# Kernel optimization log

Measured on AMD Instinct MI355X. Metric: run time of the kernel, lower is better.

The kernel has to match this reference:

```python
import jax, jax.numpy as jnp
import numpy as np

B, T, D = 1, 2048, 1024
HQ, HKV, HD = 16, 4, 64
G = HQ // HKV
E, TOPK, F = 8, 2, 2752
LB = 0.01
SCALE = HD ** -0.5


def setup_inputs() -> dict:
    key = jax.random.key(0)
    ks = jax.random.split(key, 12)
    s = 0.02
    return {
        "x": jax.random.normal(ks[0], (B, T, D), jnp.float32),
        "g1": jnp.ones((D,), jnp.float32),
        "g2": jnp.ones((D,), jnp.float32),
        "wq": jax.random.normal(ks[1], (D, HQ * HD), jnp.float32) * s,
        "wk": jax.random.normal(ks[2], (D, HKV * HD), jnp.float32) * s,
        "wv": jax.random.normal(ks[3], (D, HKV * HD), jnp.float32) * s,
        "wo": jax.random.normal(ks[4], (D, D), jnp.float32) * s,
        "gate_w": jax.random.normal(ks[5], (D, E), jnp.float32) * s,
        "we_gate": jax.random.normal(ks[6], (E, D, F), jnp.float32) * s,
        "we_up": jax.random.normal(ks[7], (E, D, F), jnp.float32) * s,
        "we_down": jax.random.normal(ks[8], (E, F, D), jnp.float32) * s,
    }


def _rmsnorm(x, g, eps=1e-6):
    return x * g * jax.lax.rsqrt(jnp.mean(x * x, axis=-1, keepdims=True) + eps)


def _rope(q, k):
    # q: [B,HQ,T,HD], k: [B,HKV,T,HD]; standard rotate-half RoPE
    pos = jnp.arange(T, dtype=jnp.float32)
    inv_freq = 1.0 / (10000.0 ** (jnp.arange(0, HD, 2, dtype=jnp.float32) / HD))
    ang = pos[:, None] * inv_freq[None, :]                  # [T, HD/2]
    cos = jnp.concatenate([jnp.cos(ang), jnp.cos(ang)], -1)  # [T, HD]
    sin = jnp.concatenate([jnp.sin(ang), jnp.sin(ang)], -1)

    def rot_half(x):
        x1, x2 = jnp.split(x, 2, axis=-1)
        return jnp.concatenate([-x2, x1], axis=-1)

    def apply(x):
        return x * cos + rot_half(x) * sin
    return apply(q), apply(k)


def _attention(x, g1, wq, wk, wv, wo):
    h = _rmsnorm(x, g1)
    q = (h @ wq).reshape(B, T, HQ, HD).transpose(0, 2, 1, 3)   # [B,HQ,T,HD]
    k = (h @ wk).reshape(B, T, HKV, HD).transpose(0, 2, 1, 3)  # [B,HKV,T,HD]
    v = (h @ wv).reshape(B, T, HKV, HD).transpose(0, 2, 1, 3)
    q, k = _rope(q, k)
    qg = q.reshape(B, HKV, G, T, HD)
    # grouped scores without materializing repeated K/V
    scores = jnp.einsum('bkgtd,bksd->bkgts', qg, k) * SCALE     # [B,HKV,G,T,T]
    causal = jnp.tril(jnp.ones((T, T), bool))
    scores = jnp.where(causal, scores, jnp.float32(-jnp.inf))
    w = jax.nn.softmax(scores, axis=-1)
    o = jnp.einsum('bkgts,bksd->bkgtd', w, v)                  # [B,HKV,G,T,HD]
    o = o.reshape(B, HQ, T, HD).transpose(0, 2, 1, 3).reshape(B, T, D)
    return o @ wo


def _moe(x, g2, gate_w, we_gate, we_up, we_down):
    h = _rmsnorm(x, g2).reshape(B * T, D)                      # [N,D]
    N = B * T
    logits = h @ gate_w                                        # [N,E]
    probs = jax.nn.softmax(logits, axis=-1)
    topv, topi = jax.lax.top_k(probs, TOPK)                    # [N,TOPK]
    topv = topv / (topv.sum(-1, keepdims=True) + 1e-8)
    # dense combine weights [N,E]: same math as masked per-expert dispatch
    combine = jnp.zeros((N, E), h.dtype).at[jnp.arange(N)[:, None], topi].add(topv)
    gh = jnp.einsum('nd,edf->enf', h, we_gate)
    up = jnp.einsum('nd,edf->enf', h, we_up)
    y = jnp.einsum('enf,efd->end', jax.nn.silu(gh) * up, we_down)
    out = jnp.einsum('end,ne->nd', y, combine).reshape(B, T, D)
    # load-balancing aux loss
    frac = jnp.zeros((E,), probs.dtype).at[topi.reshape(-1)].add(1.0) / (N * TOPK)
    load = probs.mean(axis=0)
    aux = LB * E * jnp.sum(frac * load)
    return out, aux


def reference(x, g1, g2, wq, wk, wv, wo, gate_w, we_gate, we_up, we_down):
    x = x + _attention(x, g1, wq, wk, wv, wo)
    moe_out, aux = _moe(x, g2, gate_w, we_gate, we_up, we_down)
    x = x + moe_out
    return x, aux
```

## Files before the change

kernel.cpp:

```cpp
#include <hip/hip_runtime.h>
#include <cstdint>

typedef __attribute__((ext_vector_type(8))) short short8;
typedef __attribute__((ext_vector_type(4))) float floatx4;
typedef __attribute__((ext_vector_type(4))) unsigned short ushort4v;
typedef unsigned short ushort;

#define T_LEN 2048
#define D_DIM 1024
#define HQn 16
#define HKVn 4
#define NE 8
#define FF 2752
#define NTOK 2048
#define NSLOT 4096
#define ATT_SCALE 0.125f
#define GATE_TPB 16

__device__ inline ushort f2bf(float f) {
  union { float f; unsigned int i; } v; v.f = f;
  unsigned int r = v.i + 0x7fffu + ((v.i >> 16) & 1u);
  return (ushort)(r >> 16);
}
__device__ inline float bf2f(ushort h) {
  union { unsigned int i; float f; } v; v.i = ((unsigned int)h) << 16;
  return v.f;
}
__device__ inline void split8(const float* v, short8& hi, short8& lo) {
#pragma unroll
  for (int i = 0; i < 8; i++) {
    ushort h = f2bf(v[i]);
    hi[i] = (short)h;
    lo[i] = (short)f2bf(v[i] - bf2f(h));
  }
}
__device__ inline floatx4 mfma16(short8 a, short8 b, floatx4 c) {
  return __builtin_amdgcn_mfma_f32_16x16x32_bf16(a, b, c, 0, 0, 0);
}
#define DMA16(g, l)                                                              \
  __builtin_amdgcn_global_load_lds((const __attribute__((address_space(1))) void*)(g), \
                                   (__attribute__((address_space(3))) void*)(l), 16, 0, 0)

__global__ __launch_bounds__(256) void k_cvtT(const float* __restrict__ src,
                                              ushort* __restrict__ dst, int R, int C) {
  __shared__ float tile[32][33];
  size_t sb = (size_t)blockIdx.z * R * C;
  const float* s = src + sb;
  ushort* d = dst + sb;
  int r0 = blockIdx.y * 32, c0 = blockIdx.x * 32;
  int tc = threadIdx.x & 31, tr = threadIdx.x >> 5;
#pragma unroll
  for (int i = 0; i < 4; i++)
    tile[tr + i * 8][tc] = s[(size_t)(r0 + tr + i * 8) * C + c0 + tc];
  __syncthreads();
#pragma unroll
  for (int i = 0; i < 4; i++) {
    int cc = tr + i * 8;
    d[(size_t)(c0 + cc) * R + r0 + tc] = f2bf(tile[tc][cc]);
  }
}

__global__ __launch_bounds__(256) void k_cvtT2(const float* __restrict__ src,
                                               ushort* __restrict__ dh,
                                               ushort* __restrict__ dl, int R, int C) {
  __shared__ float tile[32][33];
  int r0 = blockIdx.y * 32, c0 = blockIdx.x * 32;
  int tc = threadIdx.x & 31, tr = threadIdx.x >> 5;
#pragma unroll
  for (int i = 0; i < 4; i++)
    tile[tr + i * 8][tc] = src[(size_t)(r0 + tr + i * 8) * C + c0 + tc];
  __syncthreads();
#pragma unroll
  for (int i = 0; i < 4; i++) {
    int cc = tr + i * 8;
    float v = tile[tc][cc];
    ushort h = f2bf(v);
    dh[(size_t)(c0 + cc) * R + r0 + tc] = h;
    dl[(size_t)(c0 + cc) * R + r0 + tc] = f2bf(v - bf2f(h));
  }
}

__global__ __launch_bounds__(256) void k_rmsnorm2(const float* __restrict__ x,
                                                  const float* __restrict__ g,
                                                  ushort* __restrict__ oh,
                                                  ushort* __restrict__ ol) {
  int row = blockIdx.x;
  int t = threadIdx.x;
  const float4* x4 = (const float4*)(x + (size_t)row * D_DIM);
  float4 v = x4[t];
  float ss = v.x * v.x + v.y * v.y + v.z * v.z + v.w * v.w;
#pragma unroll
  for (int off = 32; off; off >>= 1) ss += __shfl_xor(ss, off, 64);
  __shared__ float red[4];
  if ((t & 63) == 0) red[t >> 6] = ss;
  __syncthreads();
  float tot = red[0] + red[1] + red[2] + red[3];
  float sc = rsqrtf(tot * (1.0f / D_DIM) + 1e-6f);
  const float4* g4 = (const float4*)g;
  float4 gv = g4[t];
  float vals[4] = {v.x * gv.x * sc, v.y * gv.y * sc, v.z * gv.z * sc, v.w * gv.w * sc};
  ushort4v h4, l4;
#pragma unroll
  for (int i = 0; i < 4; i++) {
    ushort h = f2bf(vals[i]);
    h4[i] = h;
    l4[i] = f2bf(vals[i] - bf2f(h));
  }
  *(ushort4v*)(oh + (size_t)row * D_DIM + t * 4) = h4;
  *(ushort4v*)(ol + (size_t)row * D_DIM + t * 4) = l4;
}

__global__ __launch_bounds__(256) void k_sgemm(const ushort* __restrict__ Ahg,
                                               const ushort* __restrict__ Alg,
                                               const ushort* __restrict__ Bhg,
                                               const ushort* __restrict__ Blg,
                                               float* __restrict__ C,
                                               const float* __restrict__ res,
                                               int N, int K) {
  __shared__ __align__(16) ushort Ah[2048], Al[2048], Bh[4096], Bl[4096];
  int tid = threadIdx.x;
  int m0 = blockIdx.y * 64, n0 = blockIdx.x * 128;
  int wave = tid >> 6, lane = tid & 63, quad = lane >> 4, l15 = lane & 15;
  int wm = (wave >> 1) * 32, wn = (wave & 1) * 64;
  floatx4 acc[2][4];
#pragma unroll
  for (int i = 0; i < 2; i++)
#pragma unroll
    for (int j = 0; j < 4; j++) acc[i][j] = (floatx4){0.f, 0.f, 0.f, 0.f};
  const ushort* src[6];
  ushort* dst[6];
  int srow = lane >> 2;
  int kc = ((lane & 3) ^ ((lane >> 3) & 3)) * 8;
#pragma unroll
  for (int j = 0; j < 6; j++) {
    int c = wave * 6 + j;
    if (c < 4) {
      src[j] = Ahg + (size_t)(m0 + c * 16 + srow) * K + kc;
      dst[j] = Ah + c * 512;
    } else if (c < 8) {
      src[j] = Alg + (size_t)(m0 + (c - 4) * 16 + srow) * K + kc;
      dst[j] = Al + (c - 4) * 512;
    } else if (c < 16) {
      src[j] = Bhg + (size_t)(n0 + (c - 8) * 16 + srow) * K + kc;
      dst[j] = Bh + (c - 8) * 512;
    } else {
      src[j] = Blg + (size_t)(n0 + (c - 16) * 16 + srow) * K + kc;
      dst[j] = Bl + (c - 16) * 512;
    }
  }
  for (int k0 = 0; k0 < K; k0 += 32) {
#pragma unroll
    for (int j = 0; j < 6; j++) DMA16(src[j] + k0, dst[j]);
    __syncthreads();
    short8 ah[2], al[2], bh[4], bl[4];
#pragma unroll
    for (int mt = 0; mt < 2; mt++) {
      int ar = wm + mt * 16 + l15;
      int sw = (quad ^ ((ar >> 1) & 3)) * 8;
      ah[mt] = *(short8*)&Ah[ar * 32 + sw];
      al[mt] = *(short8*)&Al[ar * 32 + sw];
    }
#pragma unroll
    for (int nt = 0; nt < 4; nt++) {
      int br = wn + nt * 16 + l15;
      int sw = (quad ^ ((br >> 1) & 3)) * 8;
      bh[nt] = *(short8*)&Bh[br * 32 + sw];
      bl[nt] = *(short8*)&Bl[br * 32 + sw];
    }
#pragma unroll
    for (int mt = 0; mt < 2; mt++)
#pragma unroll
      for (int nt = 0; nt < 4; nt++) {
        acc[mt][nt] = mfma16(ah[mt], bh[nt], acc[mt][nt]);
        acc[mt][nt] = mfma16(ah[mt], bl[nt], acc[mt][nt]);
        acc[mt][nt] = mfma16(al[mt], bh[nt], acc[mt][nt]);
      }
    __syncthreads();
  }
#pragma unroll
  for (int mt = 0; mt < 2; mt++) {
    int row = m0 + wm + mt * 16 + quad * 4;
#pragma unroll
    for (int nt = 0; nt < 4; nt++) {
      int col = n0 + wn + nt * 16 + l15;
#pragma unroll
      for (int r = 0; r < 4; r++) {
        float v = acc[mt][nt][r];
        if (res) v += res[(size_t)(row + r) * N + col];
        C[(size_t)(row + r) * N + col] = v;
      }
    }
  }
}

__global__ __launch_bounds__(256) void k_rope_cvt(const float* __restrict__ qkvf,
                                                  ushort* __restrict__ qhi,
                                                  ushort* __restrict__ qlo,
                                                  ushort* __restrict__ khi,
                                                  ushort* __restrict__ klo) {
  int t = blockIdx.x;
  const float* row = qkvf + (size_t)t * 1536;
  for (int it = threadIdx.x; it < (HQn + HKVn) * 32; it += 256) {
    int hh = it >> 5, i = it & 31;
    float inv = powf(10000.0f, -(float)i / 32.0f);
    float ang = (float)t * inv;
    float c = cosf(ang), s = sinf(ang);
    const float* p;
    ushort *dh, *dl;
    size_t base;
    if (hh < HQn) {
      p = row + hh * 64;
      base = ((size_t)hh * T_LEN + t) * 64;
      dh = qhi; dl = qlo;
    } else {
      int h2 = hh - HQn;
      p = row + 1024 + h2 * 64;
      base = ((size_t)h2 * T_LEN + t) * 64;
      dh = khi; dl = klo;
    }
    float a = p[i], b = p[i + 32];
    float v0 = a * c - b * s;
    float v1 = b * c + a * s;
    ushort h0 = f2bf(v0);
    dh[base + i] = h0;
    dl[base + i] = f2bf(v0 - bf2f(h0));
    ushort h1 = f2bf(v1);
    dh[base + i + 32] = h1;
    dl[base + i + 32] = f2bf(v1 - bf2f(h1));
  }
}

__global__ __launch_bounds__(256) void k_vT(const float* __restrict__ qkvf,
                                            ushort* __restrict__ vbth,
                                            ushort* __restrict__ vbtl) {
  __shared__ float tile[32][33];
  int t0 = blockIdx.x * 32;
  int dh = blockIdx.y;
  int col0 = 1280 + dh * 32;
  int tc = threadIdx.x & 31, tr = threadIdx.x >> 5;
#pragma unroll
  for (int i = 0; i < 4; i++)
    tile[tr + i * 8][tc] = qkvf[(size_t)(t0 + tr + i * 8) * 1536 + col0 + tc];
  __syncthreads();
#pragma unroll
  for (int i = 0; i < 4; i++) {
    int dd = tr + i * 8;
    float v = tile[tc][dd];
    ushort h = f2bf(v);
    size_t idx = (size_t)(dh * 32 + dd) * T_LEN + t0 + tc;
    vbth[idx] = h;
    vbtl[idx] = f2bf(v - bf2f(h));
  }
}

__global__ __launch_bounds__(256) void k_attn(const ushort* __restrict__ qhi,
                                              const ushort* __restrict__ qlo,
                                              const ushort* __restrict__ khi,
                                              const ushort* __restrict__ klo,
                                              const ushort* __restrict__ vbth,
                                              const ushort* __restrict__ vbtl,
                                              ushort* __restrict__ obh,
                                              ushort* __restrict__ obl) {
  __shared__ __align__(16) ushort Kh[4096], Kl[4096], Vh[4096], Vl[4096];
  __shared__ ushort Psh[4 * 16 * 72], Psl[4 * 16 * 72];
  int qh = blockIdx.y, kvh = qh >> 2;
  int tid = threadIdx.x, wave = tid >> 6, lane = tid & 63;
  int quad = lane >> 4, l15 = lane & 15;
  int sx = l15 >> 1;
  int rlb = lane >> 3;
  int csb = (lane & 7) ^ (lane >> 4);
#pragma unroll 1
  for (int hf = 0; hf < 2; hf++) {
    int xt = hf ? (31 - (int)blockIdx.x) : (int)blockIdx.x;
    int r0 = xt * 64;
    const ushort* qbh_ = qhi + ((size_t)qh * T_LEN + r0 + wave * 16 + l15) * 64;
    const ushort* qbl_ = qlo + ((size_t)qh * T_LEN + r0 + wave * 16 + l15) * 64;
    short8 aqh0 = *(const short8*)&qbh_[quad * 8];
    short8 aqh1 = *(const short8*)&qbh_[32 + quad * 8];
    short8 aql0 = *(const short8*)&qbl_[quad * 8];
    short8 aql1 = *(const short8*)&qbl_[32 + quad * 8];
    floatx4 oacc[4];
#pragma unroll
    for (int nt = 0; nt < 4; nt++) oacc[nt] = (floatx4){0.f, 0.f, 0.f, 0.f};
    float mrun[4], lrun[4];
#pragma unroll
    for (int r = 0; r < 4; r++) { mrun[r] = -INFINITY; lrun[r] = 0.f; }
    for (int cc = 0; cc <= xt; cc++) {
      __syncthreads();
      if (wave < 2) {
        const ushort* G = (wave == 0) ? khi : klo;
        ushort* L = (wave == 0) ? Kh : Kl;
        size_t rbase = (size_t)kvh * T_LEN + cc * 64;
#pragma unroll
        for (int i = 0; i < 8; i++) {
          int ch = csb ^ ((i & 1) * 4);
          DMA16(G + (rbase + i * 8 + rlb) * 64 + ch * 8, L + i * 512);
        }
      } else {
        const ushort* G = (wave == 2) ? vbth : vbtl;
        ushort* L = (wave == 2) ? Vh : Vl;
#pragma unroll
        for (int i = 0; i < 8; i++) {
          int ch = csb ^ ((i & 1) * 4);
          DMA16(G + ((size_t)(kvh * 64 + i * 8 + rlb)) * T_LEN + cc * 64 + ch * 8,
                L + i * 512);
        }
      }
      __syncthreads();
      floatx4 s[4];
#pragma unroll
      for (int nt = 0; nt < 4; nt++) {
        int row = nt * 16 + l15;
        short8 bh0 = *(short8*)&Kh[row * 64 + (quad ^ sx) * 8];
        short8 bh1 = *(short8*)&Kh[row * 64 + ((4 + quad) ^ sx) * 8];
        short8 bl0 = *(short8*)&Kl[row * 64 + (quad ^ sx) * 8];
        short8 bl1 = *(short8*)&Kl[row * 64 + ((4 + quad) ^ sx) * 8];
        floatx4 z = (floatx4){0.f, 0.f, 0.f, 0.f};
        z = mfma16(aqh0, bh0, z);
        z = mfma16(aqh1, bh1, z);
        z = mfma16(aqh0, bl0, z);
        z = mfma16(aqh1, bl1, z);
        z = mfma16(aql0, bh0, z);
        z = mfma16(aql1, bh1, z);
        s[nt] = z;
      }
      int rowg0 = r0 + wave * 16 + quad * 4;
#pragma unroll
      for (int nt = 0; nt < 4; nt++) {
        int colg = cc * 64 + nt * 16 + l15;
#pragma unroll
        for (int r = 0; r < 4; r++) {
          float v = s[nt][r] * ATT_SCALE;
          s[nt][r] = (colg > rowg0 + r) ? -INFINITY : v;
        }
      }
      float mnew[4], alpha[4], psum[4];
#pragma unroll
      for (int r = 0; r < 4; r++) {
        float mx = fmaxf(fmaxf(s[0][r], s[1][r]), fmaxf(s[2][r], s[3][r]));
#pragma unroll
        for (int off = 1; off < 16; off <<= 1) mx = fmaxf(mx, __shfl_xor(mx, off, 64));
        mnew[r] = fmaxf(mrun[r], mx);
        psum[r] = 0.f;
      }
#pragma unroll
      for (int nt = 0; nt < 4; nt++)
#pragma unroll
        for (int r = 0; r < 4; r++) {
          float p = __expf(s[nt][r] - mnew[r]);
          s[nt][r] = p;
          psum[r] += p;
        }
#pragma unroll
      for (int r = 0; r < 4; r++) {
        float ps = psum[r];
#pragma unroll
        for (int off = 1; off < 16; off <<= 1) ps += __shfl_xor(ps, off, 64);
        alpha[r] = __expf(mrun[r] - mnew[r]);
        lrun[r] = lrun[r] * alpha[r] + ps;
        mrun[r] = mnew[r];
      }
#pragma unroll
      for (int nt = 0; nt < 4; nt++)
#pragma unroll
        for (int r = 0; r < 4; r++) oacc[nt][r] *= alpha[r];
#pragma unroll
      for (int nt = 0; nt < 4; nt++)
#pragma unroll
        for (int r = 0; r < 4; r++) {
          float p = s[nt][r];
          ushort ph = f2bf(p);
          Psh[wave * 1152 + (quad * 4 + r) * 72 + nt * 16 + l15] = ph;
          Psl[wave * 1152 + (quad * 4 + r) * 72 + nt * 16 + l15] = f2bf(p - bf2f(ph));
        }
      short8 aph0 = *(short8*)&Psh[wave * 1152 + l15 * 72 + quad * 8];
      short8 aph1 = *(short8*)&Psh[wave * 1152 + l15 * 72 + 32 + quad * 8];
      short8 apl0 = *(short8*)&Psl[wave * 1152 + l15 * 72 + quad * 8];
      short8 apl1 = *(short8*)&Psl[wave * 1152 + l15 * 72 + 32 + quad * 8];
#pragma unroll
      for (int nt = 0; nt < 4; nt++) {
        int row = nt * 16 + l15;
        short8 bvh0 = *(short8*)&Vh[row * 64 + (quad ^ sx) * 8];
        short8 bvh1 = *(short8*)&Vh[row * 64 + ((4 + quad) ^ sx) * 8];
        short8 bvl0 = *(short8*)&Vl[row * 64 + (quad ^ sx) * 8];
        short8 bvl1 = *(short8*)&Vl[row * 64 + ((4 + quad) ^ sx) * 8];
        oacc[nt] = mfma16(aph0, bvh0, oacc[nt]);
        oacc[nt] = mfma16(aph1, bvh1, oacc[nt]);
        oacc[nt] = mfma16(aph0, bvl0, oacc[nt]);
        oacc[nt] = mfma16(aph1, bvl1, oacc[nt]);
        oacc[nt] = mfma16(apl0, bvh0, oacc[nt]);
        oacc[nt] = mfma16(apl1, bvh1, oacc[nt]);
      }
    }
#pragma unroll
    for (int nt = 0; nt < 4; nt++)
#pragma unroll
      for (int r = 0; r < 4; r++) {
        int rowg = r0 + wave * 16 + quad * 4 + r;
        float v = oacc[nt][r] / lrun[r];
        ushort h = f2bf(v);
        size_t idx = (size_t)rowg * D_DIM + qh * 64 + nt * 16 + l15;
        obh[idx] = h;
        obl[idx] = f2bf(v - bf2f(h));
      }
  }
}

__global__ __launch_bounds__(256) void k_gate(const float* __restrict__ x1,
                                              const float* __restrict__ g2,
                                              const float* __restrict__ gw,
                                              int* __restrict__ counts,
                                              int* __restrict__ ids,
                                              float* __restrict__ wts,
                                              float* __restrict__ load_sum) {
  __shared__ float lsum[NE];
  __shared__ int lcount[NE];
  __shared__ int lbase[NE];
  __shared__ int ltok[GATE_TPB * 2];
  __shared__ int lexp[GATE_TPB * 2];
  __shared__ float lwt[GATE_TPB * 2];
  int tid = threadIdx.x, wave = tid >> 6, lane = tid & 63;
  if (tid < NE) { lsum[tid] = 0.f; lcount[tid] = 0; }
  __syncthreads();
  int t0 = blockIdx.x * GATE_TPB;
#pragma unroll
  for (int tt = 0; tt < GATE_TPB / 4; tt++) {
    int tloc = tt * 4 + wave;
    int token = t0 + tloc;
    const float* xp = x1 + (size_t)token * D_DIM;
    float acc[NE] = {};
    float ss = 0.f;
    for (int d = lane; d < D_DIM; d += 64) {
      float xv = xp[d];
      ss += xv * xv;
      float hv = xv * g2[d];
#pragma unroll
      for (int e = 0; e < NE; e++) acc[e] += hv * gw[d * NE + e];
    }
#pragma unroll
    for (int off = 32; off; off >>= 1) ss += __shfl_xor(ss, off, 64);
#pragma unroll
    for (int e = 0; e < NE; e++)
#pragma unroll
      for (int off = 32; off; off >>= 1) acc[e] += __shfl_xor(acc[e], off, 64);
    if (lane == 0) {
      float sc = rsqrtf(ss * (1.0f / D_DIM) + 1e-6f);
      float mx = -1e30f;
#pragma unroll
      for (int e = 0; e < NE; e++) { acc[e] *= sc; mx = fmaxf(mx, acc[e]); }
      float p[NE], sum = 0.f;
#pragma unroll
      for (int e = 0; e < NE; e++) { p[e] = expf(acc[e] - mx); sum += p[e]; }
#pragma unroll
      for (int e = 0; e < NE; e++) p[e] /= sum;
      int i1 = 0;
#pragma unroll
      for (int e = 1; e < NE; e++) if (acc[e] > acc[i1]) i1 = e;
      int i2 = (i1 == 0) ? 1 : 0;
#pragma unroll
      for (int e = 0; e < NE; e++) if (e != i1 && acc[e] > acc[i2]) i2 = e;
      float denom = p[i1] + p[i2] + 1e-8f;
      int slot = tloc * 2;
      lexp[slot] = i1; ltok[slot] = token; lwt[slot] = p[i1] / denom;
      lexp[slot + 1] = i2; ltok[slot + 1] = token; lwt[slot + 1] = p[i2] / denom;
      atomicAdd(&lcount[i1], 1);
      atomicAdd(&lcount[i2], 1);
#pragma unroll
      for (int e = 0; e < NE; e++) atomicAdd(&lsum[e], p[e]);
    }
  }
  __syncthreads();
  if (tid < NE) {
    lbase[tid] = atomicAdd(&counts[tid], lcount[tid]);
    atomicAdd(&load_sum[tid], lsum[tid]);
    lcount[tid] = 0;
  }
  __syncthreads();
  if (tid < GATE_TPB * 2) {
    int e = lexp[tid];
    int off = atomicAdd(&lcount[e], 1);
    int pos = lbase[e] + off;
    ids[e * NTOK + pos] = ltok[tid];
    wts[e * NTOK + pos] = lwt[tid];
  }
}

__global__ void k_offsets(const int* __restrict__ counts, int* __restrict__ offsets) {
  if (threadIdx.x == 0 && blockIdx.x == 0) {
    int s = 0;
    for (int e = 0; e < NE; e++) { offsets[e] = s; s += counts[e]; }
  }
}

__global__ __launch_bounds__(256) void k_moe_gateup(const ushort* __restrict__ h,
                                                    const ushort* __restrict__ wgT,
                                                    const ushort* __restrict__ wuT,
                                                    const int* __restrict__ ids,
                                                    const float* __restrict__ wts,
                                                    const int* __restrict__ counts,
                                                    const int* __restrict__ offsets,
                                                    ushort* __restrict__ act) {
  int e = blockIdx.z;
  int cnt = counts[e];
  int m0 = blockIdx.y * 128;
  if (m0 >= cnt) return;
  int n0 = blockIdx.x * 64;
  __shared__ __align__(16) ushort As[4096], Bg[2048], Bu[2048];
  __shared__ int toks[128];
  __shared__ float wrow[128];
  int tid = threadIdx.x;
  if (tid < 128) {
    int mm = m0 + tid;
    toks[tid] = (mm < cnt) ? ids[e * NTOK + mm] : 0;
    wrow[tid] = (mm < cnt) ? wts[e * NTOK + mm] : 0.f;
  }
  __syncthreads();
  int wave = tid >> 6, lane = tid & 63, quad = lane >> 4, l15 = lane & 15;
  int wm = (wave >> 1) * 64, wn = (wave & 1) * 32;
  const ushort* Wg = wgT + (size_t)e * FF * D_DIM;
  const ushort* Wu = wuT + (size_t)e * FF * D_DIM;
  const ushort* src[4];
  ushort* dst[4];
  int srow = lane >> 2;
  int kc = ((lane & 3) ^ ((lane >> 3) & 3)) * 8;
#pragma unroll
  for (int j = 0; j < 4; j++) {
    int c = wave * 4 + j;
    if (c < 8) {
      src[j] = h + (size_t)toks[c * 16 + srow] * D_DIM + kc;
      dst[j] = As + c * 512;
    } else if (c < 12) {
      src[j] = Wg + (size_t)(n0 + (c - 8) * 16 + srow) * D_DIM + kc;
      dst[j] = Bg + (c - 8) * 512;
    } else {
      src[j] = Wu + (size_t)(n0 + (c - 12) * 16 + srow) * D_DIM + kc;
      dst[j] = Bu + (c - 12) * 512;
    }
  }
  floatx4 accg[4][2], accu[4][2];
#pragma unroll
  for (int i = 0; i < 4; i++)
#pragma unroll
    for (int j = 0; j < 2; j++) {
      accg[i][j] = (floatx4){0.f, 0.f, 0.f, 0.f};
      accu[i][j] = (floatx4){0.f, 0.f, 0.f, 0.f};
    }
  for (int k0 = 0; k0 < D_DIM; k0 += 32) {
#pragma unroll
    for (int j = 0; j < 4; j++) DMA16(src[j] + k0, dst[j]);
    __syncthreads();
    short8 aF[4], bgF[2], buF[2];
#pragma unroll
    for (int mt = 0; mt < 4; mt++) {
      int ar = wm + mt * 16 + l15;
      int sw = (quad ^ ((ar >> 1) & 3)) * 8;
      aF[mt] = *(short8*)&As[ar * 32 + sw];
    }
#pragma unroll
    for (int nt = 0; nt < 2; nt++) {
      int br = wn + nt * 16 + l15;
      int sw = (quad ^ ((br >> 1) & 3)) * 8;
      bgF[nt] = *(short8*)&Bg[br * 32 + sw];
      buF[nt] = *(short8*)&Bu[br * 32 + sw];
    }
#pragma unroll
    for (int mt = 0; mt < 4; mt++)
#pragma unroll
      for (int nt = 0; nt < 2; nt++) {
        accg[mt][nt] = mfma16(aF[mt], bgF[nt], accg[mt][nt]);
        accu[mt][nt] = mfma16(aF[mt], buF[nt], accu[mt][nt]);
      }
    __syncthreads();
  }
  int aoff = offsets[e];
#pragma unroll
  for (int mt = 0; mt < 4; mt++) {
    int mrow = wm + mt * 16 + quad * 4;
#pragma unroll
    for (int nt = 0; nt < 2; nt++) {
      int col = n0 + wn + nt * 16 + l15;
#pragma unroll
      for (int r = 0; r < 4; r++) {
        int ml = mrow + r;
        if (m0 + ml < cnt) {
          float g = accg[mt][nt][r];
          float u = accu[mt][nt][r];
          float sil = g / (1.f + __expf(-g));
          act[(size_t)(aoff + m0 + ml) * FF + col] = f2bf(sil * u * wrow[ml]);
        }
      }
    }
  }
}

__global__ __launch_bounds__(256) void k_moe_down(const ushort* __restrict__ act,
                                                  const ushort* __restrict__ wdT,
                                                  const int* __restrict__ ids,
                                                  const int* __restrict__ counts,
                                                  const int* __restrict__ offsets,
                                                  float* __restrict__ moe_acc) {
  int e = blockIdx.z & 7;
  int kh = blockIdx.z >> 3;
  int cnt = counts[e];
  int m0 = blockIdx.y * 128;
  if (m0 >= cnt) return;
  int n0 = blockIdx.x * 128;
  __shared__ __align__(16) ushort As[4096], Bs[4096];
  __shared__ int toks[128];
  int tid = threadIdx.x;
  if (tid < 128) {
    int mm = m0 + tid;
    toks[tid] = (mm < cnt) ? ids[e * NTOK + mm] : 0;
  }
  __syncthreads();
  int wave = tid >> 6, lane = tid & 63, quad = lane >> 4, l15 = lane & 15;
  int wm = (wave >> 1) * 64, wn = (wave & 1) * 64;
  int aoff = offsets[e];
  const ushort* Wd = wdT + (size_t)e * D_DIM * FF;
  const ushort* src[4];
  ushort* dst[4];
  int srow = lane >> 2;
  int kc = ((lane & 3) ^ ((lane >> 3) & 3)) * 8;
#pragma unroll
  for (int j = 0; j < 4; j++) {
    int c = wave * 4 + j;
    if (c < 8) {
      src[j] = act + (size_t)(aoff + m0 + c * 16 + srow) * FF + kc;
      dst[j] = As + c * 512;
    } else {
      src[j] = Wd + (size_t)(n0 + (c - 8) * 16 + srow) * FF + kc;
      dst[j] = Bs + (c - 8) * 512;
    }
  }
  floatx4 acc[4][4];
#pragma unroll
  for (int i = 0; i < 4; i++)
#pragma unroll
    for (int j = 0; j < 4; j++) acc[i][j] = (floatx4){0.f, 0.f, 0.f, 0.f};
  int kbeg = kh * 1376;
  for (int k0 = kbeg; k0 < kbeg + 1376; k0 += 32) {
#pragma unroll
    for (int j = 0; j < 4; j++) DMA16(src[j] + k0, dst[j]);
    __syncthreads();
    short8 aF[4], bF[4];
#pragma unroll
    for (int mt = 0; mt < 4; mt++) {
      int ar = wm + mt * 16 + l15;
      int sw = (quad ^ ((ar >> 1) & 3)) * 8;
      aF[mt] = *(short8*)&As[ar * 32 + sw];
    }
#pragma unroll
    for (int nt = 0; nt < 4; nt++) {
      int br = wn + nt * 16 + l15;
      int sw = (quad ^ ((br >> 1) & 3)) * 8;
      bF[nt] = *(short8*)&Bs[br * 32 + sw];
    }
#pragma unroll
    for (int mt = 0; mt < 4; mt++)
#pragma unroll
      for (int nt = 0; nt < 4; nt++) acc[mt][nt] = mfma16(aF[mt], bF[nt], acc[mt][nt]);
    __syncthreads();
  }
#pragma unroll
  for (int mt = 0; mt < 4; mt++) {
    int mrow = wm + mt * 16 + quad * 4;
#pragma unroll
    for (int nt = 0; nt < 4; nt++) {
      int col = n0 + wn + nt * 16 + l15;
#pragma unroll
      for (int r = 0; r < 4; r++) {
        int ml = mrow + r;
        if (m0 + ml < cnt)
          atomicAdd(&moe_acc[(size_t)toks[ml] * D_DIM + col], acc[mt][nt][r]);
      }
    }
  }
}

__global__ __launch_bounds__(256) void k_add(const float* __restrict__ a,
                                             const float* __restrict__ b,
                                             float* __restrict__ o) {
  int i = blockIdx.x * 256 + threadIdx.x;
  float4 va = ((const float4*)a)[i];
  float4 vb = ((const float4*)b)[i];
  float4 vo;
  vo.x = va.x + vb.x; vo.y = va.y + vb.y; vo.z = va.z + vb.z; vo.w = va.w + vb.w;
  ((float4*)o)[i] = vo;
}

__global__ void k_aux(const int* __restrict__ counts, const float* __restrict__ load_sum,
                      float* __restrict__ out_aux) {
  if (threadIdx.x == 0 && blockIdx.x == 0) {
    float s = 0.f;
    for (int e = 0; e < NE; e++)
      s += ((float)counts[e] / (float)NSLOT) * (load_sum[e] / (float)NTOK);
    *out_aux = 0.01f * (float)NE * s;
  }
}

extern "C" void kernel_launch(void* const* d_in, const int* in_sizes, int n_in,
                              void* d_out, int out_size, void* d_ws, size_t ws_size,
                              hipStream_t stream) {
  const float* x = (const float*)d_in[0];
  const float* g1 = (const float*)d_in[1];
  const float* g2 = (const float*)d_in[2];
  const float* wq = (const float*)d_in[3];
  const float* wk = (const float*)d_in[4];
  const float* wv = (const float*)d_in[5];
  const float* wo = (const float*)d_in[6];
  const float* gate_w = (const float*)d_in[7];
  const float* we_gate = (const float*)d_in[8];
  const float* we_up = (const float*)d_in[9];
  const float* we_down = (const float*)d_in[10];
  float* out = (float*)d_out;

  char* w = (char*)d_ws;
  size_t o = 0;
  auto alloc = [&](size_t bytes) -> char* {
    char* p = w + o;
    o = (o + bytes + 255) & ~(size_t)255;
    return p;
  };
  ushort* h1h = (ushort*)alloc((size_t)NTOK * D_DIM * 2);
  ushort* h1l = (ushort*)alloc((size_t)NTOK * D_DIM * 2);
  float* qkvf = (float*)alloc((size_t)NTOK * 1536 * 4);
  ushort* qhi = (ushort*)alloc((size_t)HQn * T_LEN * 64 * 2);
  ushort* qlo = (ushort*)alloc((size_t)HQn * T_LEN * 64 * 2);
  ushort* khi = (ushort*)alloc((size_t)HKVn * T_LEN * 64 * 2);
  ushort* klo = (ushort*)alloc((size_t)HKVn * T_LEN * 64 * 2);
  ushort* vbth = (ushort*)alloc((size_t)HKVn * 64 * T_LEN * 2);
  ushort* vbtl = (ushort*)alloc((size_t)HKVn * 64 * T_LEN * 2);
  ushort* obh = (ushort*)alloc((size_t)NTOK * D_DIM * 2);
  ushort* obl = (ushort*)alloc((size_t)NTOK * D_DIM * 2);
  float* x1 = (float*)alloc((size_t)NTOK * D_DIM * 4);
  float* moe_acc = (float*)alloc((size_t)NTOK * D_DIM * 4);
  ushort* act = (ushort*)alloc((size_t)(NSLOT + 128) * FF * 2);
  ushort* qkvwTh = (ushort*)alloc((size_t)1536 * 1024 * 2);
  ushort* qkvwTl = (ushort*)alloc((size_t)1536 * 1024 * 2);
  ushort* woTh = (ushort*)alloc((size_t)1024 * 1024 * 2);
  ushort* woTl = (ushort*)alloc((size_t)1024 * 1024 * 2);
  ushort* h2h = (ushort*)alloc((size_t)NTOK * D_DIM * 2);
  ushort* h2l = (ushort*)alloc((size_t)NTOK * D_DIM * 2);
  ushort* wgT = (ushort*)alloc((size_t)NE * FF * D_DIM * 2);
  ushort* wuT = (ushort*)alloc((size_t)NE * FF * D_DIM * 2);
  ushort* wdT = (ushort*)alloc((size_t)NE * D_DIM * FF * 2);
  int* counts = (int*)alloc(NE * 4);
  int* offsets = (int*)alloc(NE * 4);
  float* load_sum = (float*)alloc(NE * 4);
  int* ids = (int*)alloc((size_t)NE * NTOK * 4);
  float* wts = (float*)alloc((size_t)NE * NTOK * 4);

  hipMemsetAsync(moe_acc, 0, (size_t)NTOK * D_DIM * 4, stream);
  hipMemsetAsync(counts, 0, 768, stream);

  k_cvtT2<<<dim3(32, 32), 256, 0, stream>>>(wq, qkvwTh, qkvwTl, 1024, 1024);
  k_cvtT2<<<dim3(8, 32), 256, 0, stream>>>(wk, qkvwTh + (size_t)1024 * 1024,
                                           qkvwTl + (size_t)1024 * 1024, 1024, 256);
  k_cvtT2<<<dim3(8, 32), 256, 0, stream>>>(wv, qkvwTh + (size_t)1280 * 1024,
                                           qkvwTl + (size_t)1280 * 1024, 1024, 256);
  k_cvtT2<<<dim3(32, 32), 256, 0, stream>>>(wo, woTh, woTl, 1024, 1024);
  k_cvtT<<<dim3(86, 32, 8), 256, 0, stream>>>(we_gate, wgT, 1024, 2752);
  k_cvtT<<<dim3(86, 32, 8), 256, 0, stream>>>(we_up, wuT, 1024, 2752);
  k_cvtT<<<dim3(32, 86, 8), 256, 0, stream>>>(we_down, wdT, 2752, 1024);

  k_rmsnorm2<<<NTOK, 256, 0, stream>>>(x, g1, h1h, h1l);
  k_sgemm<<<dim3(12, 32), 256, 0, stream>>>(h1h, h1l, qkvwTh, qkvwTl, qkvf, nullptr,
                                            1536, 1024);
  k_rope_cvt<<<T_LEN, 256, 0, stream>>>(qkvf, qhi, qlo, khi, klo);
  k_vT<<<dim3(64, 8), 256, 0, stream>>>(qkvf, vbth, vbtl);
  k_attn<<<dim3(16, 16), 256, 0, stream>>>(qhi, qlo, khi, klo, vbth, vbtl, obh, obl);
  k_sgemm<<<dim3(8, 32), 256, 0, stream>>>(obh, obl, woTh, woTl, x1, x, 1024, 1024);

  k_rmsnorm2<<<NTOK, 256, 0, stream>>>(x1, g2, h2h, h2l);
  k_gate<<<NTOK / GATE_TPB, 256, 0, stream>>>(x1, g2, gate_w, counts, ids, wts, load_sum);
  k_offsets<<<1, 1, 0, stream>>>(counts, offsets);
  k_moe_gateup<<<dim3(43, 16, 8), 256, 0, stream>>>(h2h, wgT, wuT, ids, wts, counts,
                                                    offsets, act);
  k_moe_down<<<dim3(8, 16, 16), 256, 0, stream>>>(act, wdT, ids, counts, offsets, moe_acc);
  k_add<<<(NTOK * D_DIM) / (256 * 4), 256, 0, stream>>>(x1, moe_acc, out);
  k_aux<<<1, 1, 0, stream>>>(counts, load_sum, out + (size_t)NTOK * D_DIM);
}
```

Before: 709.9 us.

## Double-buffer LDS tiles in GEMM and MoE kernels to overlap loads with MFMA

Replaces the single LDS tile in the sgemm, MoE gate/up and MoE down kernels with two ping-pong buffers. Each iteration issues the async global-to-LDS copy for the next K slice before computing on the current one, so only one barrier per step remains. This aims to hide global memory latency behind MFMA work. It doubles LDS per block, which may reduce the number of resident blocks per CU.

```diff
diff --git a/kernel.cpp b/kernel.cpp
--- a/kernel.cpp
+++ b/kernel.cpp
@@ -117,7 +117,7 @@
                                                float* __restrict__ C,
                                                const float* __restrict__ res,
                                                int N, int K) {
-  __shared__ __align__(16) ushort Ah[2048], Al[2048], Bh[4096], Bl[4096];
+  __shared__ __align__(16) ushort L0[12288], L1[12288];
   int tid = threadIdx.x;
   int m0 = blockIdx.y * 64, n0 = blockIdx.x * 128;
   int wave = tid >> 6, lane = tid & 63, quad = lane >> 4, l15 = lane & 15;
@@ -128,7 +128,7 @@
 #pragma unroll
     for (int j = 0; j < 4; j++) acc[i][j] = (floatx4){0.f, 0.f, 0.f, 0.f};
   const ushort* src[6];
-  ushort* dst[6];
+  int off[6];
   int srow = lane >> 2;
   int kc = ((lane & 3) ^ ((lane >> 3) & 3)) * 8;
 #pragma unroll
@@ -136,22 +136,27 @@
     int c = wave * 6 + j;
     if (c < 4) {
       src[j] = Ahg + (size_t)(m0 + c * 16 + srow) * K + kc;
-      dst[j] = Ah + c * 512;
+      off[j] = c * 512;
     } else if (c < 8) {
       src[j] = Alg + (size_t)(m0 + (c - 4) * 16 + srow) * K + kc;
-      dst[j] = Al + (c - 4) * 512;
+      off[j] = 2048 + (c - 4) * 512;
     } else if (c < 16) {
       src[j] = Bhg + (size_t)(n0 + (c - 8) * 16 + srow) * K + kc;
-      dst[j] = Bh + (c - 8) * 512;
+      off[j] = 4096 + (c - 8) * 512;
     } else {
       src[j] = Blg + (size_t)(n0 + (c - 16) * 16 + srow) * K + kc;
-      dst[j] = Bl + (c - 16) * 512;
-    }
-  }
-  for (int k0 = 0; k0 < K; k0 += 32) {
-#pragma unroll
-    for (int j = 0; j < 6; j++) DMA16(src[j] + k0, dst[j]);
-    __syncthreads();
+      off[j] = 8192 + (c - 16) * 512;
+    }
+  }
+  auto stage = [&](ushort* Ld, int k0) {
+#pragma unroll
+    for (int j = 0; j < 6; j++) DMA16(src[j] + k0, Ld + off[j]);
+  };
+  auto compute = [&](const ushort* Ld) {
+    const ushort* Ah = Ld;
+    const ushort* Al = Ld + 2048;
+    const ushort* Bh = Ld + 4096;
+    const ushort* Bl = Ld + 8192;
     short8 ah[2], al[2], bh[4], bl[4];
 #pragma unroll
     for (int mt = 0; mt < 2; mt++) {
@@ -175,17 +180,29 @@
         acc[mt][nt] = mfma16(ah[mt], bl[nt], acc[mt][nt]);
         acc[mt][nt] = mfma16(al[mt], bh[nt], acc[mt][nt]);
       }
+  };
+  int nt = K >> 5;
+  stage(L0, 0);
+  __syncthreads();
+  for (int t = 0; t < nt; t++) {
+    if ((t & 1) == 0) {
+      if (t + 1 < nt) stage(L1, (t + 1) << 5);
+      compute(L0);
+    } else {
+      if (t + 1 < nt) stage(L0, (t + 1) << 5);
+      compute(L1);
+    }
     __syncthreads();
   }
 #pragma unroll
   for (int mt = 0; mt < 2; mt++) {
     int row = m0 + wm + mt * 16 + quad * 4;
 #pragma unroll
-    for (int nt = 0; nt < 4; nt++) {
-      int col = n0 + wn + nt * 16 + l15;
+    for (int nt2 = 0; nt2 < 4; nt2++) {
+      int col = n0 + wn + nt2 * 16 + l15;
 #pragma unroll
       for (int r = 0; r < 4; r++) {
-        float v = acc[mt][nt][r];
+        float v = acc[mt][nt2][r];
         if (res) v += res[(size_t)(row + r) * N + col];
         C[(size_t)(row + r) * N + col] = v;
       }
@@ -505,7 +522,7 @@
   int m0 = blockIdx.y * 128;
   if (m0 >= cnt) return;
   int n0 = blockIdx.x * 64;
-  __shared__ __align__(16) ushort As[4096], Bg[2048], Bu[2048];
+  __shared__ __align__(16) ushort L0[8192], L1[8192];
   __shared__ int toks[128];
   __shared__ float wrow[128];
   int tid = threadIdx.x;
@@ -520,7 +537,7 @@
   const ushort* Wg = wgT + (size_t)e * FF * D_DIM;
   const ushort* Wu = wuT + (size_t)e * FF * D_DIM;
   const ushort* src[4];
-  ushort* dst[4];
+  int off[4];
   int srow = lane >> 2;
   int kc = ((lane & 3) ^ ((lane >> 3) & 3)) * 8;
 #pragma unroll
@@ -528,13 +545,13 @@
     int c = wave * 4 + j;
     if (c < 8) {
       src[j] = h + (size_t)toks[c * 16 + srow] * D_DIM + kc;
-      dst[j] = As + c * 512;
+      off[j] = c * 512;
     } else if (c < 12) {
       src[j] = Wg + (size_t)(n0 + (c - 8) * 16 + srow) * D_DIM + kc;
-      dst[j] = Bg + (c - 8) * 512;
+      off[j] = 4096 + (c - 8) * 512;
     } else {
       src[j] = Wu + (size_t)(n0 + (c - 12) * 16 + srow) * D_DIM + kc;
-      dst[j] = Bu + (c - 12) * 512;
+      off[j] = 6144 + (c - 12) * 512;
     }
   }
   floatx4 accg[4][2], accu[4][2];
@@ -545,10 +562,14 @@
       accg[i][j] = (floatx4){0.f, 0.f, 0.f, 0.f};
       accu[i][j] = (floatx4){0.f, 0.f, 0.f, 0.f};
     }
-  for (int k0 = 0; k0 < D_DIM; k0 += 32) {
-#pragma unroll
-    for (int j = 0; j < 4; j++) DMA16(src[j] + k0, dst[j]);
-    __syncthreads();
+  auto stage = [&](ushort* Ld, int k0) {
+#pragma unroll
+    for (int j = 0; j < 4; j++) DMA16(src[j] + k0, Ld + off[j]);
+  };
+  auto compute = [&](const ushort* Ld) {
+    const ushort* As = Ld;
+    const ushort* Bg = Ld + 4096;
+    const ushort* Bu = Ld + 6144;
     short8 aF[4], bgF[2], buF[2];
 #pragma unroll
     for (int mt = 0; mt < 4; mt++) {
@@ -570,6 +591,17 @@
         accg[mt][nt] = mfma16(aF[mt], bgF[nt], accg[mt][nt]);
         accu[mt][nt] = mfma16(aF[mt], buF[nt], accu[mt][nt]);
       }
+  };
+  stage(L0, 0);
+  __syncthreads();
+  for (int t = 0; t < 32; t++) {
+    if ((t & 1) == 0) {
+      if (t + 1 < 32) stage(L1, (t + 1) << 5);
+      compute(L0);
+    } else {
+      if (t + 1 < 32) stage(L0, (t + 1) << 5);
+      compute(L1);
+    }
     __syncthreads();
   }
   int aoff = offsets[e];
@@ -605,7 +637,7 @@
   int m0 = blockIdx.y * 128;
   if (m0 >= cnt) return;
   int n0 = blockIdx.x * 128;
-  __shared__ __align__(16) ushort As[4096], Bs[4096];
+  __shared__ __align__(16) ushort L0[8192], L1[8192];
   __shared__ int toks[128];
   int tid = threadIdx.x;
   if (tid < 128) {
@@ -618,7 +650,7 @@
   int aoff = offsets[e];
   const ushort* Wd = wdT + (size_t)e * D_DIM * FF;
   const ushort* src[4];
-  ushort* dst[4];
+  int off[4];
   int srow = lane >> 2;
   int kc = ((lane & 3) ^ ((lane >> 3) & 3)) * 8;
 #pragma unroll
@@ -626,10 +658,10 @@
     int c = wave * 4 + j;
     if (c < 8) {
       src[j] = act + (size_t)(aoff + m0 + c * 16 + srow) * FF + kc;
-      dst[j] = As + c * 512;
+      off[j] = c * 512;
     } else {
       src[j] = Wd + (size_t)(n0 + (c - 8) * 16 + srow) * FF + kc;
-      dst[j] = Bs + (c - 8) * 512;
+      off[j] = 4096 + (c - 8) * 512;
     }
   }
   floatx4 acc[4][4];
@@ -637,11 +669,13 @@
   for (int i = 0; i < 4; i++)
 #pragma unroll
     for (int j = 0; j < 4; j++) acc[i][j] = (floatx4){0.f, 0.f, 0.f, 0.f};
-  int kbeg = kh * 1376;
-  for (int k0 = kbeg; k0 < kbeg + 1376; k0 += 32) {
-#pragma unroll
-    for (int j = 0; j < 4; j++) DMA16(src[j] + k0, dst[j]);
-    __syncthreads();
+  auto stage = [&](ushort* Ld, int k0) {
+#pragma unroll
+    for (int j = 0; j < 4; j++) DMA16(src[j] + k0, Ld + off[j]);
+  };
+  auto compute = [&](const ushort* Ld) {
+    const ushort* As = Ld;
+    const ushort* Bs = Ld + 4096;
     short8 aF[4], bF[4];
 #pragma unroll
     for (int mt = 0; mt < 4; mt++) {
@@ -659,19 +693,32 @@
     for (int mt = 0; mt < 4; mt++)
 #pragma unroll
       for (int nt = 0; nt < 4; nt++) acc[mt][nt] = mfma16(aF[mt], bF[nt], acc[mt][nt]);
+  };
+  int kbeg = kh * 1376;
+  int nt = 43;
+  stage(L0, kbeg);
+  __syncthreads();
+  for (int t = 0; t < nt; t++) {
+    if ((t & 1) == 0) {
+      if (t + 1 < nt) stage(L1, kbeg + ((t + 1) << 5));
+      compute(L0);
+    } else {
+      if (t + 1 < nt) stage(L0, kbeg + ((t + 1) << 5));
+      compute(L1);
+    }
     __syncthreads();
   }
 #pragma unroll
   for (int mt = 0; mt < 4; mt++) {
     int mrow = wm + mt * 16 + quad * 4;
 #pragma unroll
-    for (int nt = 0; nt < 4; nt++) {
-      int col = n0 + wn + nt * 16 + l15;
+    for (int nt2 = 0; nt2 < 4; nt2++) {
+      int col = n0 + wn + nt2 * 16 + l15;
 #pragma unroll
       for (int r = 0; r < 4; r++) {
         int ml = mrow + r;
         if (m0 + ml < cnt)
-          atomicAdd(&moe_acc[(size_t)toks[ml] * D_DIM + col], acc[mt][nt][r]);
+          atomicAdd(&moe_acc[(size_t)toks[ml] * D_DIM + col], acc[mt][nt2][r]);
       }
     }
   }
```

Result: no change. 710.9 us (+0.1%).
